# Kernel optimization log

Hardware: AMD Instinct MI355X
Metric: run time of the kernel (lower is better)

## Reference

```python
import jax, jax.numpy as jnp
import numpy as np

DA_ALPHA = 0.1
DA_LAMDA = 0.5
MAT_DIFF_SCALE = 0.001
KERNEL_MUL = 2.0
KERNEL_NUM = 5

B = 4096
D = 1024
N_CLASSES = 40
K_DIM = 64  # trans_feat is [B, 64, 64]


def setup_inputs() -> dict:
    key = jax.random.key(0)
    k1, k2, k3, k4, k5 = jax.random.split(key, 5)
    logits = jax.random.normal(k1, (B, N_CLASSES), dtype=jnp.float32)
    pred = jax.nn.log_softmax(logits, axis=-1)  # NLL expects log-probs
    target = jax.random.randint(k2, (B,), 0, N_CLASSES, dtype=jnp.int64)
    trans_feat = jax.random.normal(k3, (B, K_DIM, K_DIM), dtype=jnp.float32)
    feature_dense = jax.random.normal(k4, (B, D), dtype=jnp.float32)
    feature_sparse = jax.random.normal(k5, (B, D), dtype=jnp.float32)
    return {
        "pred": pred,
        "target": target,
        "trans_feat": trans_feat,
        "feature_dense": feature_dense,
        "feature_sparse": feature_sparse,
    }


def _nll_loss(pred, target):
    # F.nll_loss with mean reduction: -mean(pred[i, target[i]])
    return -jnp.mean(jnp.take_along_axis(pred, target[:, None], axis=1))


def _feature_transform_regularizer(trans):
    # PointNet: mean over batch of ||I - T T^T||_F
    k = trans.shape[-1]
    eye = jnp.eye(k, dtype=trans.dtype)
    diff = eye - jnp.einsum("bij,bkj->bik", trans, trans)
    return jnp.mean(jnp.sqrt(jnp.sum(diff * diff, axis=(1, 2))))


def _gaussian_kernel_sum(source, target):
    n_samples = source.shape[0] + target.shape[0]
    total = jnp.concatenate([source, target], axis=0)  # [N, D]
    sq = jnp.sum(total * total, axis=-1)  # [N]
    # pairwise squared L2 via GEMM instead of N x N x D broadcast
    l2 = sq[:, None] + sq[None, :] - 2.0 * (total @ total.T)
    l2 = jnp.maximum(l2, 0.0)  # numerical floor (math is >= 0)
    # bandwidth computed from detached distances (torch uses .data)
    bandwidth = jax.lax.stop_gradient(jnp.sum(l2)) / (n_samples ** 2 - n_samples)
    bandwidth = bandwidth / (KERNEL_MUL ** (KERNEL_NUM // 2))
    kernel = jnp.zeros_like(l2)
    for i in range(KERNEL_NUM):
        kernel = kernel + jnp.exp(-l2 / (bandwidth * (KERNEL_MUL ** i)))
    return kernel


def reference(pred, target, trans_feat, feature_dense, feature_sparse):
    loss = _nll_loss(pred, target)
    mat_diff_loss = _feature_transform_regularizer(trans_feat)
    bsz = pred.shape[0]
    kernels = _gaussian_kernel_sum(feature_dense, feature_sparse)  # [2B, 2B]
    xx = jnp.mean(kernels[:bsz, :bsz])
    yy = jnp.mean(kernels[bsz:, bsz:])
    xy = jnp.mean(kernels[:bsz, bsz:])
    yx = jnp.mean(kernels[bsz:, :bsz])
    mmd_loss = xx + yy - xy - yx
    total_loss = DA_ALPHA * loss + mat_diff_loss * MAT_DIFF_SCALE + DA_LAMDA * mmd_loss
    return total_loss
```

## Files before the change

### kernel.cpp

```cpp
#include <hip/hip_runtime.h>
#include <math.h>

#define B_ROWS 4096
#define DIM    1024
#define NTOT   8192
#define NCLS   40
#define TILES2 32
#define NTILE  528
#define NQUAR  64
#define NFULL  512
#define NMATD  512
#define NNLL   8
#define NMAIN  (NQUAR + NFULL + NMATD + NNLL)

typedef __attribute__((ext_vector_type(8))) short bf16x8;
typedef __attribute__((ext_vector_type(4))) float f32x4;

#define WS_TOT_BYTE_OFF 36896

#define MFMA16(d, x, y) d = __builtin_amdgcn_mfma_f32_16x16x32_bf16(x, y, d, 0, 0, 0)

__device__ __forceinline__ unsigned short f2bf(float f) {
  unsigned int u = __float_as_uint(f);
  u += 0x7fffu + ((u >> 16) & 1u);
  return (unsigned short)(u >> 16);
}

__device__ __forceinline__ void async16(const void* g, void* l) {
  __builtin_amdgcn_global_load_lds(
      (const __attribute__((address_space(1))) unsigned int*)g,
      (__attribute__((address_space(3))) unsigned int*)l, 16, 0, 0);
}

__device__ __forceinline__ float wave_sum(float v) {
  v += __shfl_xor(v, 32);
  v += __shfl_xor(v, 16);
  v += __shfl_xor(v, 8);
  v += __shfl_xor(v, 4);
  v += __shfl_xor(v, 2);
  v += __shfl_xor(v, 1);
  return v;
}

__device__ __forceinline__ void decode_tile(int p, int& bi_o, int& bj_o) {
  int bi = (int)((2 * TILES2 + 1 -
                  sqrtf((float)((2 * TILES2 + 1) * (2 * TILES2 + 1) - 8 * p))) * 0.5f);
  if (bi < 0) bi = 0;
  if (bi >= TILES2) bi = TILES2 - 1;
  int start = bi * (2 * TILES2 - bi + 1) / 2;
  while (p < start) { --bi; start = bi * (2 * TILES2 - bi + 1) / 2; }
  while (p >= start + (TILES2 - bi)) { start += TILES2 - bi; ++bi; }
  bi_o = bi; bj_o = bi + (p - start);
}

__global__ __launch_bounds__(512) void prep_k(const float* __restrict__ dense,
                                              const float* __restrict__ sparse,
                                              float* __restrict__ W,
                                              unsigned short* __restrict__ tot) {
  float* colsum = W + 8;
  float* sq = W + 1032;
  const int t = threadIdx.x;
  const int lane = t & 63, wave = t >> 6;
  const int blk = blockIdx.x;
  __shared__ float colsum_l[1024];
  __shared__ float red[8];
  colsum_l[t * 2] = 0.f;
  colsum_l[t * 2 + 1] = 0.f;

  float c[4][4];
  #pragma unroll
  for (int j = 0; j < 4; ++j)
    #pragma unroll
    for (int x = 0; x < 4; ++x) c[j][x] = 0.f;

  float rowtot = 0.f;
  const int rbase = blk * 32 + wave * 4;
  for (int i = 0; i < 4; ++i) {
    const int r = rbase + i;
    const float* src = (r < B_ROWS) ? dense + (size_t)r * DIM
                                    : sparse + (size_t)(r - B_ROWS) * DIM;
    float sp = 0.f;
    #pragma unroll
    for (int j = 0; j < 4; ++j) {
      float4 v = ((const float4*)src)[lane + 64 * j];
      c[j][0] += v.x; c[j][1] += v.y; c[j][2] += v.z; c[j][3] += v.w;
      sp += v.x * v.x + v.y * v.y + v.z * v.z + v.w * v.w;
      ushort4 o;
      o.x = f2bf(v.x); o.y = f2bf(v.y); o.z = f2bf(v.z); o.w = f2bf(v.w);
      *(ushort4*)(tot + (size_t)r * DIM + (lane + 64 * j) * 4) = o;
    }
    sp = wave_sum(sp);
    if (lane == 0) { sq[r] = sp; rowtot += sp; }
  }
  if (lane == 0) red[wave] = rowtot;

  __syncthreads();
  #pragma unroll
  for (int j = 0; j < 4; ++j)
    #pragma unroll
    for (int x = 0; x < 4; ++x)
      atomicAdd(&colsum_l[4 * lane + 256 * j + x], c[j][x]);
  __syncthreads();
  #pragma unroll
  for (int x = 0; x < 2; ++x) {
    const int g = (t * 2 + x + blk * 64) & 1023;
    atomicAdd(&colsum[g], colsum_l[g]);
  }
  if (t == 0) {
    float s = 0.f;
    #pragma unroll
    for (int w = 0; w < 8; ++w) s += red[w];
    atomicAdd(&W[2], s);
  }
}


struct SmemMain {
  short A[4][8192];
  short B[4][8192];
  float sqA[256], sqB[256], red[8];
};

__device__ void gram_full_body(int p, const unsigned short* __restrict__ tot,
                               float* __restrict__ W, SmemMain& sm) {
  const float* sq = W + 1032;
  const float* colsum = W + 8;
  const int t = threadIdx.x;
  const int lane = t & 63, wave = t >> 6;
  const int wr = wave >> 2, wc = wave & 3;

  int bi, bj;
  decode_tile(p, bi, bj);

  const int r0 = t >> 2;
  const int sg = (t & 3) ^ ((r0 >> 1) & 3);
  const unsigned short* gA0 = tot + (size_t)(bi * 256 + r0) * DIM + sg * 8;
  const unsigned short* gA1 = gA0 + (size_t)128 * DIM;
  const unsigned short* gB0 = tot + (size_t)(bj * 256 + r0) * DIM + sg * 8;
  const unsigned short* gB1 = gB0 + (size_t)128 * DIM;
  const int ldo0 = t * 8, ldo1 = t * 8 + 4096;

  auto stageA = [&](int kt, short* sl) {
    const size_t ko = (size_t)kt * 32;
    async16(gA0 + ko, sl + ldo0);
    async16(gA1 + ko, sl + ldo1);
  };
  auto stageB = [&](int kt, short* sl) {
    const size_t ko = (size_t)kt * 32;
    async16(gB0 + ko, sl + ldo0);
    async16(gB1 + ko, sl + ldo1);
  };

  stageA(0, &sm.A[0][0]); stageB(0, &sm.B[0][0]);
  stageA(1, &sm.A[1][0]); stageB(1, &sm.B[1][0]);
  stageA(2, &sm.A[2][0]); stageB(2, &sm.B[2][0]);

  if (t < 256) sm.sqA[t] = sq[bi * 256 + t];
  else         sm.sqB[t - 256] = sq[bj * 256 + (t - 256)];
  float csp = 0.f;
  #pragma unroll
  for (int j = 0; j < 16; ++j) { float v = colsum[lane + 64 * j]; csp += v * v; }
  csp = wave_sum(csp);
  double sumdots = (double)csp;
  double sum_sq = (double)W[2];
  double sumL2 = 2.0 * (double)NTOT * sum_sq - 2.0 * sumdots;
  double bwv = sumL2 / ((double)NTOT * (double)NTOT - (double)NTOT);
  const float cexp16 = (float)(4.0 / bwv) * 0.0625f;

  f32x4 acc[8][4];
  #pragma unroll
  for (int m = 0; m < 8; ++m)
    #pragma unroll
    for (int n = 0; n < 4; ++n) acc[m][n] = (f32x4)(0.f);

  const int q = lane >> 4;
  const int fr = lane & 15;
  const int rb = (q ^ ((fr >> 1) & 3)) << 4;
  const int aoff = (wr * 128 + fr) * 64 + rb;
  const int boff = (wc * 64 + fr) * 64 + rb;

  asm volatile("s_waitcnt vmcnt(8)" ::: "memory");
  __builtin_amdgcn_s_barrier();

  for (int u = 0; u < 8; ++u) {
    #pragma unroll
    for (int j = 0; j < 4; ++j) {
      const int kt = u * 4 + j;
      const char* cA = (const char*)&sm.A[j][0];
      const char* cB = (const char*)&sm.B[j][0];
      short* stA = &sm.A[(j + 3) & 3][0];
      short* stB = &sm.B[(j + 3) & 3][0];
      const bool st = (kt < 29);

      bf16x8 a[4], b[4];

      #pragma unroll
      for (int m = 0; m < 4; ++m) a[m] = *(const bf16x8*)(cA + aoff + m * 1024);
      #pragma unroll
      for (int n = 0; n < 4; ++n) b[n] = *(const bf16x8*)(cB + boff + n * 1024);
      if (st) stageA(kt + 3, stA);
      __builtin_amdgcn_s_barrier();
      asm volatile("s_waitcnt lgkmcnt(0)" ::: "memory");
      __builtin_amdgcn_s_setprio(1);
      #pragma unroll
      for (int m = 0; m < 4; ++m)
        #pragma unroll
        for (int n = 0; n < 4; ++n) MFMA16(acc[m][n], a[m], b[n]);
      __builtin_amdgcn_s_setprio(0);
      __builtin_amdgcn_s_barrier();

      #pragma unroll
      for (int m = 0; m < 4; ++m) a[m] = *(const bf16x8*)(cA + aoff + (4 + m) * 1024);
      if (st) stageB(kt + 3, stB);
      __builtin_amdgcn_s_barrier();
      asm volatile("s_waitcnt lgkmcnt(0)" ::: "memory");
      __builtin_amdgcn_s_setprio(1);
      #pragma unroll
      for (int m = 0; m < 4; ++m)
        #pragma unroll
        for (int n = 0; n < 4; ++n) MFMA16(acc[4 + m][n], a[m], b[n]);
      __builtin_amdgcn_s_setprio(0);
      if (kt < 29)       { asm volatile("s_waitcnt vmcnt(8)" ::: "memory"); }
      else if (kt == 29) { asm volatile("s_waitcnt vmcnt(4)" ::: "memory"); }
      else if (kt == 30) { asm volatile("s_waitcnt vmcnt(0)" ::: "memory"); }
      __builtin_amdgcn_s_barrier();
    }
  }

  float s = 0.f;
  const int crow = (lane >> 4) * 4;
  #pragma unroll
  for (int m = 0; m < 8; ++m) {
    #pragma unroll
    for (int n = 0; n < 4; ++n) {
      #pragma unroll
      for (int r = 0; r < 4; ++r) {
        int il = wr * 128 + 16 * m + crow + r;
        int jl = wc * 64 + 16 * n + fr;
        float l2 = sm.sqA[il] + sm.sqB[jl] - 2.f * acc[m][n][r];
        l2 = fmaxf(l2, 0.f);
        float k4 = __expf(-l2 * cexp16);
        float k3 = k4 * k4;
        float k2 = k3 * k3;
        float k1 = k2 * k2;
        float k0 = k1 * k1;
        s += k0 + k1 + k2 + k3 + k4;
      }
    }
  }
  s = wave_sum(s);
  if (lane == 0) sm.red[wave] = s;
  __syncthreads();
  if (t == 0) {
    float ts = 0.f;
    #pragma unroll
    for (int w = 0; w < 8; ++w) ts += sm.red[w];
    int idx; float wgt;
    if (bi == bj)      { idx = (bi < 16) ? 3 : 4; wgt = 1.f; }
    else if (bj < 16)  { idx = 3; wgt = 2.f; }
    else if (bi >= 16) { idx = 4; wgt = 2.f; }
    else               { idx = 5; wgt = 2.f; }
    atomicAdd(&W[idx], wgt * ts);
  }
}

__device__ void gram_quarter_body(int p, int quad,
                                  const unsigned short* __restrict__ tot,
                                  float* __restrict__ W, SmemMain& sm) {
  const float* sq = W + 1032;
  const float* colsum = W + 8;
  const int t = threadIdx.x;
  const int lane = t & 63, wave = t >> 6;
  const int wr = wave >> 2, wc = wave & 3;

  int bi, bj;
  decode_tile(p, bi, bj);
  const int h = quad >> 1, v = quad & 1;
  const int rA = bi * 256 + h * 128;
  const int rB = bj * 256 + v * 128;

  const int r0 = t >> 2;
  const int sg = (t & 3) ^ ((r0 >> 1) & 3);
  const unsigned short* gA0 = tot + (size_t)(rA + r0) * DIM + sg * 8;
  const unsigned short* gB0 = tot + (size_t)(rB + r0) * DIM + sg * 8;
  const int ldo = t * 8;

  auto stage = [&](int kt, short* sa, short* sb) {
    const size_t ko = (size_t)kt * 32;
    async16(gA0 + ko, sa + ldo);
    async16(gB0 + ko, sb + ldo);
  };

  stage(0, &sm.A[0][0], &sm.B[0][0]);
  stage(1, &sm.A[1][0], &sm.B[1][0]);
  stage(2, &sm.A[2][0], &sm.B[2][0]);

  if (t < 128)      sm.sqA[t] = sq[rA + t];
  else if (t < 256) sm.sqB[t - 128] = sq[rB + (t - 128)];
  float csp = 0.f;
  #pragma unroll
  for (int j = 0; j < 16; ++j) { float v2 = colsum[lane + 64 * j]; csp += v2 * v2; }
  csp = wave_sum(csp);
  double sumdots = (double)csp;
  double sum_sq = (double)W[2];
  double sumL2 = 2.0 * (double)NTOT * sum_sq - 2.0 * sumdots;
  double bwv = sumL2 / ((double)NTOT * (double)NTOT - (double)NTOT);
  const float cexp16 = (float)(4.0 / bwv) * 0.0625f;

  f32x4 acc[4][2];
  #pragma unroll
  for (int m = 0; m < 4; ++m)
    #pragma unroll
    for (int n = 0; n < 2; ++n) acc[m][n] = (f32x4)(0.f);

  const int q = lane >> 4;
  const int fr = lane & 15;
  const int rb = (q ^ ((fr >> 1) & 3)) << 4;
  const int aoff = (wr * 64 + fr) * 64 + rb;
  const int boff = (wc * 32 + fr) * 64 + rb;

  asm volatile("s_waitcnt vmcnt(4)" ::: "memory");
  __builtin_amdgcn_s_barrier();

  for (int u = 0; u < 8; ++u) {
    #pragma unroll
    for (int j = 0; j < 4; ++j) {
      const int kt = u * 4 + j;
      const char* cA = (const char*)&sm.A[j][0];
      const char* cB = (const char*)&sm.B[j][0];
      short* stA = &sm.A[(j + 3) & 3][0];
      short* stB = &sm.B[(j + 3) & 3][0];

      bf16x8 a[4], b[2];
      #pragma unroll
      for (int m = 0; m < 4; ++m) a[m] = *(const bf16x8*)(cA + aoff + m * 1024);
      #pragma unroll
      for (int n = 0; n < 2; ++n) b[n] = *(const bf16x8*)(cB + boff + n * 1024);
      if (kt < 29) stage(kt + 3, stA, stB);
      __builtin_amdgcn_s_barrier();
      asm volatile("s_waitcnt lgkmcnt(0)" ::: "memory");
      __builtin_amdgcn_s_setprio(1);
      #pragma unroll
      for (int m = 0; m < 4; ++m)
        #pragma unroll
        for (int n = 0; n < 2; ++n) MFMA16(acc[m][n], a[m], b[n]);
      __builtin_amdgcn_s_setprio(0);
      if (kt < 29)       { asm volatile("s_waitcnt vmcnt(4)" ::: "memory"); }
      else if (kt == 29) { asm volatile("s_waitcnt vmcnt(2)" ::: "memory"); }
      else if (kt == 30) { asm volatile("s_waitcnt vmcnt(0)" ::: "memory"); }
      __builtin_amdgcn_s_barrier();
    }
  }

  float s = 0.f;
  const int crow = (lane >> 4) * 4;
  #pragma unroll
  for (int m = 0; m < 4; ++m) {
    #pragma unroll
    for (int n = 0; n < 2; ++n) {
      #pragma unroll
      for (int r = 0; r < 4; ++r) {
        int il = wr * 64 + 16 * m + crow + r;
        int jl = wc * 32 + 16 * n + fr;
        float l2 = sm.sqA[il] + sm.sqB[jl] - 2.f * acc[m][n][r];
        l2 = fmaxf(l2, 0.f);
        float k4 = __expf(-l2 * cexp16);
        float k3 = k4 * k4;
        float k2 = k3 * k3;
        float k1 = k2 * k2;
        float k0 = k1 * k1;
        s += k0 + k1 + k2 + k3 + k4;
      }
    }
  }
  s = wave_sum(s);
  if (lane == 0) sm.red[wave] = s;
  __syncthreads();
  if (t == 0) {
    float ts = 0.f;
    #pragma unroll
    for (int w = 0; w < 8; ++w) ts += sm.red[w];
    int idx; float wgt;
    if (bi == bj)      { idx = (bi < 16) ? 3 : 4; wgt = 1.f; }
    else if (bj < 16)  { idx = 3; wgt = 2.f; }
    else if (bi >= 16) { idx = 4; wgt = 2.f; }
    else               { idx = 5; wgt = 2.f; }
    atomicAdd(&W[idx], wgt * ts);
  }
}

__device__ void nll_body(int bid, const float* __restrict__ pred,
                         const int* __restrict__ tgt, float* __restrict__ W,
                         SmemMain& sm) {
  const int t = threadIdx.x;
  const int i = bid * 512 + t;
  float v = pred[(size_t)i * NCLS + tgt[i]];
  v = wave_sum(v);
  if ((t & 63) == 0) sm.red[t >> 6] = v;
  __syncthreads();
  if (t == 0) {
    float s = 0.f;
    #pragma unroll
    for (int w = 0; w < 8; ++w) s += sm.red[w];
    atomicAdd(&W[0], s);
  }
}

__device__ void matdiff_body(int bid, const float* __restrict__ trans,
                             float* __restrict__ W, SmemMain& sm) {
  const int t = threadIdx.x;
  const int lane = t & 63, wave = t >> 6;
  const int b = bid * 8 + wave;
  const float* Tb = trans + (size_t)b * 4096;
  const int fr = lane & 15;
  const int k8 = (lane >> 4) * 8;
  bf16x8 frag[4][2];
  #pragma unroll
  for (int m = 0; m < 4; ++m) {
    #pragma unroll
    for (int kk = 0; kk < 2; ++kk) {
      const float* p = Tb + (size_t)(16 * m + fr) * 64 + kk * 32 + k8;
      float4 u0 = *(const float4*)p;
      float4 u1 = *(const float4*)(p + 4);
      bf16x8 f;
      f[0] = (short)f2bf(u0.x); f[1] = (short)f2bf(u0.y);
      f[2] = (short)f2bf(u0.z); f[3] = (short)f2bf(u0.w);
      f[4] = (short)f2bf(u1.x); f[5] = (short)f2bf(u1.y);
      f[6] = (short)f2bf(u1.z); f[7] = (short)f2bf(u1.w);
      frag[m][kk] = f;
    }
  }
  f32x4 acc[4][4];
  #pragma unroll
  for (int m = 0; m < 4; ++m)
    #pragma unroll
    for (int n = 0; n < 4; ++n) acc[m][n] = (f32x4)(0.f);
  #pragma unroll
  for (int kk = 0; kk < 2; ++kk)
    #pragma unroll
    for (int m = 0; m < 4; ++m)
      #pragma unroll
      for (int n = 0; n < 4; ++n)
        acc[m][n] = __builtin_amdgcn_mfma_f32_16x16x32_bf16(frag[m][kk], frag[n][kk],
                                                            acc[m][n], 0, 0, 0);
  float s = 0.f;
  const int crow = (lane >> 4) * 4;
  #pragma unroll
  for (int m = 0; m < 4; ++m)
    #pragma unroll
    for (int n = 0; n < 4; ++n)
      #pragma unroll
      for (int r = 0; r < 4; ++r) {
        int grow = 16 * m + crow + r;
        int gcol = 16 * n + fr;
        float g = acc[m][n][r];
        float d = (grow == gcol) ? (1.f - g) : (-g);
        s += d * d;
      }
  s = wave_sum(s);
  if (lane == 0) sm.red[wave] = sqrtf(s);
  __syncthreads();
  if (t == 0) {
    float s8 = 0.f;
    #pragma unroll
    for (int w = 0; w < 8; ++w) s8 += sm.red[w];
    atomicAdd(&W[1], s8);
  }
}

__global__ __launch_bounds__(512, 2) void main_k(
    const float* __restrict__ pred, const int* __restrict__ tgt,
    const float* __restrict__ trans, const unsigned short* __restrict__ tot,
    float* __restrict__ W, float* __restrict__ out) {
  __shared__ SmemMain sm;
  const int blk = blockIdx.x;
  if (blk < NQUAR) {
    gram_quarter_body(512 + (blk >> 2), blk & 3, tot, W, sm);
  } else if (blk < NQUAR + NFULL) {
    const int bfull = blk - NQUAR;
    gram_full_body((bfull & 7) * 64 + (bfull >> 3), tot, W, sm);
  } else if (blk < NQUAR + NFULL + NMATD) {
    matdiff_body(blk - NQUAR - NFULL, trans, W, sm);
  } else {
    nll_body(blk - NQUAR - NFULL - NMATD, pred, tgt, W, sm);
  }

  if (threadIdx.x == 0) {
    __threadfence();
    unsigned int tk = atomicAdd((unsigned int*)(W + 7), 1u);
    if (tk == NMAIN - 1) {
      __threadfence();
      float nll = -*(volatile float*)(W + 0) / (float)B_ROWS;
      float mat =  *(volatile float*)(W + 1) / (float)B_ROWS;
      float sxx =  *(volatile float*)(W + 3);
      float syy =  *(volatile float*)(W + 4);
      float smx =  *(volatile float*)(W + 5);
      float mmd = (sxx + syy - smx) / ((float)B_ROWS * (float)B_ROWS);
      out[0] = 0.1f * nll + 0.001f * mat + 0.5f * mmd;
    }
  }
}

extern "C" void kernel_launch(void* const* d_in, const int* in_sizes, int n_in,
                              void* d_out, int out_size, void* d_ws, size_t ws_size,
                              hipStream_t stream) {
  const float* pred   = (const float*)d_in[0];
  const int*   tgt    = (const int*)d_in[1];
  const float* trans  = (const float*)d_in[2];
  const float* dense  = (const float*)d_in[3];
  const float* sparse = (const float*)d_in[4];
  float* W = (float*)d_ws;
  unsigned short* tot = (unsigned short*)((char*)d_ws + WS_TOT_BYTE_OFF);
  float* out = (float*)d_out;

  hipMemsetAsync(W, 0, 1032 * sizeof(float), stream);
  prep_k<<<dim3(256), dim3(512), 0, stream>>>(dense, sparse, W, tot);
  main_k<<<dim3(NMAIN), dim3(512), 0, stream>>>(pred, tgt, trans, tot, W, out);
}
```

Baseline: 156.9 us.

## Restructure GEMM main loop into double-buffered two-k-slice steps with quadrant MFMA phases

Replaces the 4-stage, 3-deep async prefetch pipeline over single 32-wide k slices with a ping-pong scheme that computes two k slices per step from one half of the LDS buffers while the next two slices load into the other half. Each step is split into four MFMA quadrant phases (A-low/B-low, A-low/B-high, A-high/B-low, A-high/B-high) with LDS reads and global staging interleaved between them. The aim is fewer loop iterations and barriers per unit of k and more MFMA work per synchronisation. The trade-off is a shallower prefetch distance with a full vmcnt(0) wait at the end of every step, plus higher register pressure from holding the lo/hi fragments for two slices at once.

```diff
diff --git a/kernel.cpp b/kernel.cpp
--- a/kernel.cpp
+++ b/kernel.cpp
@@ -140,20 +140,19 @@
   const unsigned short* gB1 = gB0 + (size_t)128 * DIM;
   const int ldo0 = t * 8, ldo1 = t * 8 + 4096;
 
-  auto stageA = [&](int kt, short* sl) {
-    const size_t ko = (size_t)kt * 32;
+  auto stageA = [&](int pl, short* sl) {
+    const size_t ko = (size_t)pl * 32;
     async16(gA0 + ko, sl + ldo0);
     async16(gA1 + ko, sl + ldo1);
   };
-  auto stageB = [&](int kt, short* sl) {
-    const size_t ko = (size_t)kt * 32;
+  auto stageB = [&](int pl, short* sl) {
+    const size_t ko = (size_t)pl * 32;
     async16(gB0 + ko, sl + ldo0);
     async16(gB1 + ko, sl + ldo1);
   };
 
-  stageA(0, &sm.A[0][0]); stageB(0, &sm.B[0][0]);
-  stageA(1, &sm.A[1][0]); stageB(1, &sm.B[1][0]);
-  stageA(2, &sm.A[2][0]); stageB(2, &sm.B[2][0]);
+  stageA(0, &sm.A[0][0]); stageA(1, &sm.A[1][0]);
+  stageB(0, &sm.B[0][0]); stageB(1, &sm.B[1][0]);
 
   if (t < 256) sm.sqA[t] = sq[bi * 256 + t];
   else         sm.sqB[t - 256] = sq[bj * 256 + (t - 256)];
@@ -179,52 +178,92 @@
   const int aoff = (wr * 128 + fr) * 64 + rb;
   const int boff = (wc * 64 + fr) * 64 + rb;
 
-  asm volatile("s_waitcnt vmcnt(8)" ::: "memory");
+  asm volatile("s_waitcnt vmcnt(0)" ::: "memory");
   __builtin_amdgcn_s_barrier();
 
-  for (int u = 0; u < 8; ++u) {
-    #pragma unroll
-    for (int j = 0; j < 4; ++j) {
-      const int kt = u * 4 + j;
-      const char* cA = (const char*)&sm.A[j][0];
-      const char* cB = (const char*)&sm.B[j][0];
-      short* stA = &sm.A[(j + 3) & 3][0];
-      short* stB = &sm.B[(j + 3) & 3][0];
-      const bool st = (kt < 29);
-
-      bf16x8 a[4], b[4];
-
-      #pragma unroll
-      for (int m = 0; m < 4; ++m) a[m] = *(const bf16x8*)(cA + aoff + m * 1024);
-      #pragma unroll
-      for (int n = 0; n < 4; ++n) b[n] = *(const bf16x8*)(cB + boff + n * 1024);
-      if (st) stageA(kt + 3, stA);
-      __builtin_amdgcn_s_barrier();
-      asm volatile("s_waitcnt lgkmcnt(0)" ::: "memory");
-      __builtin_amdgcn_s_setprio(1);
-      #pragma unroll
-      for (int m = 0; m < 4; ++m)
-        #pragma unroll
-        for (int n = 0; n < 4; ++n) MFMA16(acc[m][n], a[m], b[n]);
-      __builtin_amdgcn_s_setprio(0);
-      __builtin_amdgcn_s_barrier();
-
-      #pragma unroll
-      for (int m = 0; m < 4; ++m) a[m] = *(const bf16x8*)(cA + aoff + (4 + m) * 1024);
-      if (st) stageB(kt + 3, stB);
-      __builtin_amdgcn_s_barrier();
-      asm volatile("s_waitcnt lgkmcnt(0)" ::: "memory");
-      __builtin_amdgcn_s_setprio(1);
-      #pragma unroll
-      for (int m = 0; m < 4; ++m)
-        #pragma unroll
-        for (int n = 0; n < 4; ++n) MFMA16(acc[4 + m][n], a[m], b[n]);
-      __builtin_amdgcn_s_setprio(0);
-      if (kt < 29)       { asm volatile("s_waitcnt vmcnt(8)" ::: "memory"); }
-      else if (kt == 29) { asm volatile("s_waitcnt vmcnt(4)" ::: "memory"); }
-      else if (kt == 30) { asm volatile("s_waitcnt vmcnt(0)" ::: "memory"); }
-      __builtin_amdgcn_s_barrier();
-    }
+  for (int s = 0; s < 16; ++s) {
+    const int c0 = (s & 1) * 2, c1 = c0 + 1;
+    const int n0 = 2 - c0, n1 = n0 + 1;
+    const bool st = (s < 15);
+    const char* Ac0 = (const char*)&sm.A[c0][0];
+    const char* Ac1 = (const char*)&sm.A[c1][0];
+    const char* Bc0 = (const char*)&sm.B[c0][0];
+    const char* Bc1 = (const char*)&sm.B[c1][0];
+
+    bf16x8 alo[4][2], ahi[4][2], blo[2][2], bhi[2][2];
+
+    #pragma unroll
+    for (int m = 0; m < 4; ++m) {
+      alo[m][0] = *(const bf16x8*)(Ac0 + aoff + m * 1024);
+      alo[m][1] = *(const bf16x8*)(Ac1 + aoff + m * 1024);
+    }
+    #pragma unroll
+    for (int n = 0; n < 2; ++n) {
+      blo[n][0] = *(const bf16x8*)(Bc0 + boff + n * 1024);
+      blo[n][1] = *(const bf16x8*)(Bc1 + boff + n * 1024);
+    }
+    if (st) { stageA(2 * (s + 1), &sm.A[n0][0]); stageA(2 * (s + 1) + 1, &sm.A[n1][0]); }
+    __builtin_amdgcn_s_barrier();
+    asm volatile("s_waitcnt lgkmcnt(0)" ::: "memory");
+    __builtin_amdgcn_s_setprio(1);
+    #pragma unroll
+    for (int m = 0; m < 4; ++m)
+      #pragma unroll
+      for (int n = 0; n < 2; ++n) {
+        MFMA16(acc[m][n], alo[m][0], blo[n][0]);
+        MFMA16(acc[m][n], alo[m][1], blo[n][1]);
+      }
+    __builtin_amdgcn_s_setprio(0);
+    __builtin_amdgcn_s_barrier();
+
+    #pragma unroll
+    for (int n = 0; n < 2; ++n) {
+      bhi[n][0] = *(const bf16x8*)(Bc0 + boff + (2 + n) * 1024);
+      bhi[n][1] = *(const bf16x8*)(Bc1 + boff + (2 + n) * 1024);
+    }
+    if (st) { stageB(2 * (s + 1), &sm.B[n0][0]); stageB(2 * (s + 1) + 1, &sm.B[n1][0]); }
+    __builtin_amdgcn_s_barrier();
+    asm volatile("s_waitcnt lgkmcnt(0)" ::: "memory");
+    __builtin_amdgcn_s_setprio(1);
+    #pragma unroll
+    for (int m = 0; m < 4; ++m)
+      #pragma unroll
+      for (int n = 0; n < 2; ++n) {
+        MFMA16(acc[m][2 + n], alo[m][0], bhi[n][0]);
+        MFMA16(acc[m][2 + n], alo[m][1], bhi[n][1]);
+      }
+    __builtin_amdgcn_s_setprio(0);
+    __builtin_amdgcn_s_barrier();
+
+    #pragma unroll
+    for (int m = 0; m < 4; ++m) {
+      ahi[m][0] = *(const bf16x8*)(Ac0 + aoff + (4 + m) * 1024);
+      ahi[m][1] = *(const bf16x8*)(Ac1 + aoff + (4 + m) * 1024);
+    }
+    __builtin_amdgcn_s_barrier();
+    asm volatile("s_waitcnt lgkmcnt(0)" ::: "memory");
+    __builtin_amdgcn_s_setprio(1);
+    #pragma unroll
+    for (int m = 0; m < 4; ++m)
+      #pragma unroll
+      for (int n = 0; n < 2; ++n) {
+        MFMA16(acc[4 + m][n], ahi[m][0], blo[n][0]);
+        MFMA16(acc[4 + m][n], ahi[m][1], blo[n][1]);
+      }
+    __builtin_amdgcn_s_setprio(0);
+    __builtin_amdgcn_s_barrier();
+
+    __builtin_amdgcn_s_setprio(1);
+    #pragma unroll
+    for (int m = 0; m < 4; ++m)
+      #pragma unroll
+      for (int n = 0; n < 2; ++n) {
+        MFMA16(acc[4 + m][2 + n], ahi[m][0], bhi[n][0]);
+        MFMA16(acc[4 + m][2 + n], ahi[m][1], bhi[n][1]);
+      }
+    __builtin_amdgcn_s_setprio(0);
+    asm volatile("s_waitcnt vmcnt(0)" ::: "memory");
+    __builtin_amdgcn_s_barrier();
   }
 
   float s = 0.f;
```

Result: no change. 159.0 us (+1.4%).
